# Kernel tuning notes

Measured on AMD Instinct MI355X. Metric: run time of the kernel, lower is better.

Reference implementation:

```python
import jax, jax.numpy as jnp
import numpy as np

H = 1024   # hidden_dim
NH = 16    # num_heads
HD = H // NH  # head_dim = 64
B, S = 2, 2048
LN_EPS = 1e-5


def setup_inputs() -> dict:
    key = jax.random.key(0)
    ks = jax.random.split(key, 5)
    scale = 1.0 / np.sqrt(H)  # xavier-ish scale for stability
    return {
        "x": jax.random.normal(ks[0], (B, S, H), dtype=jnp.float32),
        "Wq": jax.random.normal(ks[1], (H, H), dtype=jnp.float32) * scale,
        "bq": jnp.zeros((H,), jnp.float32),
        "Wk": jax.random.normal(ks[2], (H, H), dtype=jnp.float32) * scale,
        "bk": jnp.zeros((H,), jnp.float32),
        "Wv": jax.random.normal(ks[3], (H, H), dtype=jnp.float32) * scale,
        "bv": jnp.zeros((H,), jnp.float32),
        "Wo": jax.random.normal(ks[4], (H, H), dtype=jnp.float32) * scale,
        "bo": jnp.zeros((H,), jnp.float32),
        "ln_gamma": jnp.ones((H,), jnp.float32),
        "ln_beta": jnp.zeros((H,), jnp.float32),
    }


def reference(x, Wq, bq, Wk, bk, Wv, bv, Wo, bo, ln_gamma, ln_beta):
    b, s, _ = x.shape
    # QKV projections, split heads: (b, nh, s, hd)
    def split_heads(t):
        return t.reshape(b, s, NH, HD).transpose(0, 2, 1, 3)
    Q = split_heads(x @ Wq + bq)
    K = split_heads(x @ Wk + bk)
    V = split_heads(x @ Wv + bv)
    # scaled dot-product with clamp (mask=None path)
    scores = jnp.einsum('bhqd,bhkd->bhqk', Q, K) / np.sqrt(HD).astype(np.float32)
    scores = jnp.clip(scores, -10000.0, 10000.0)
    attn = jax.nn.softmax(scores, axis=-1)
    # dropout is identity in eval mode
    ctx = jnp.einsum('bhqk,bhkd->bhqd', attn, V)
    ctx = ctx.transpose(0, 2, 1, 3).reshape(b, s, H)
    out = ctx @ Wo + bo
    # residual + LayerNorm
    y = out + x
    mu = jnp.mean(y, axis=-1, keepdims=True)
    var = jnp.mean(jnp.square(y - mu), axis=-1, keepdims=True)
    y = (y - mu) * jax.lax.rsqrt(var + LN_EPS)
    return y * ln_gamma + ln_beta
```

## Files before the change

kernel.cpp:

```cpp
#include <hip/hip_runtime.h>

typedef unsigned short u16;
typedef __attribute__((ext_vector_type(8))) short shortx8;
typedef __attribute__((ext_vector_type(4))) float floatx4;
typedef __attribute__((ext_vector_type(2))) unsigned uintx2;

#define GLD16(gp, lp) __builtin_amdgcn_global_load_lds( \
    (__attribute__((address_space(1))) void*)(gp), \
    (__attribute__((address_space(3))) void*)(lp), 16, 0, 0)

__device__ __forceinline__ u16 f2bf(float f) {
  union { float f; unsigned u; } v; v.f = f;
  unsigned r = v.u + 0x7FFFu + ((v.u >> 16) & 1u);
  return (u16)(r >> 16);
}

__device__ __forceinline__ unsigned f2bf_u32(float f) {
  union { float f; unsigned u; } v; v.f = f;
  return (v.u + 0x8000u) >> 16;
}

__global__ __launch_bounds__(256) void cast_x_kernel(const float* __restrict__ x,
                                                     u16* __restrict__ xb, int n4) {
  int i = blockIdx.x * 256 + threadIdx.x;
  if (i < n4) {
    float4 v = ((const float4*)x)[i];
    ushort4 o;
    o.x = f2bf(v.x); o.y = f2bf(v.y); o.z = f2bf(v.z); o.w = f2bf(v.w);
    ((ushort4*)xb)[i] = o;
  }
}

__global__ __launch_bounds__(256) void transpose_cast_w(const float* __restrict__ Wq,
                                                        const float* __restrict__ Wk,
                                                        const float* __restrict__ Wv,
                                                        const float* __restrict__ Wo,
                                                        u16* __restrict__ Wt) {
  __shared__ u16 tile[32][33];
  int mat = blockIdx.z;
  const float* W = (mat == 0) ? Wq : (mat == 1) ? Wk : (mat == 2) ? Wv : Wo;
  u16* dst = Wt + (size_t)mat * 1024 * 1024;
  int n0 = blockIdx.x * 32, k0 = blockIdx.y * 32;
  int tx = threadIdx.x, ty = threadIdx.y;
  for (int i = 0; i < 4; ++i)
    tile[ty + i * 8][tx] = f2bf(W[(size_t)(k0 + ty + i * 8) * 1024 + n0 + tx]);
  __syncthreads();
  for (int i = 0; i < 4; ++i)
    dst[(size_t)(n0 + ty + i * 8) * 1024 + k0 + tx] = tile[tx][ty + i * 8];
}

__device__ __forceinline__ void gemm_tile_core(const u16* __restrict__ A,
                                               const u16* __restrict__ Bt,
                                               int m0, int n0,
                                               u16* As, u16* Bs,
                                               floatx4 (&acc)[4][4]) {
  const int tid = threadIdx.x;
  const int wave = tid >> 6, lane = tid & 63;
  const int lrow = lane >> 4, lcol = lane & 15;
  const int wm = wave >> 1, wn = wave & 1;

  for (int mi = 0; mi < 4; ++mi)
    for (int ni = 0; ni < 4; ++ni)
      acc[mi][ni] = (floatx4){0.f, 0.f, 0.f, 0.f};

  const u16* ap[4];
  const u16* bp[4];
  for (int l = 0; l < 4; ++l) {
    int g = (l * 4 + wave) * 64 + lane;
    int r = g >> 3, c = g & 7;
    int cc = (c ^ (r & 7)) * 8;
    ap[l] = A + (size_t)(m0 + r) * 1024 + cc;
    bp[l] = Bt + (size_t)(n0 + r) * 1024 + cc;
  }

  for (int k0 = 0; k0 < 1024; k0 += 64) {
    __syncthreads();
    for (int l = 0; l < 4; ++l) {
      GLD16(ap[l], As + (l * 4 + wave) * 512);
      GLD16(bp[l], Bs + (l * 4 + wave) * 512);
      ap[l] += 64; bp[l] += 64;
    }
    __syncthreads();
    for (int kk = 0; kk < 2; ++kk) {
      shortx8 af[4], bf[4];
      for (int mi = 0; mi < 4; ++mi) {
        int row = wm * 64 + mi * 16 + lcol;
        int gr = (kk * 4 + lrow) ^ (row & 7);
        af[mi] = *(const shortx8*)&As[row * 64 + gr * 8];
      }
      for (int ni = 0; ni < 4; ++ni) {
        int row = wn * 64 + ni * 16 + lcol;
        int gr = (kk * 4 + lrow) ^ (row & 7);
        bf[ni] = *(const shortx8*)&Bs[row * 64 + gr * 8];
      }
      for (int mi = 0; mi < 4; ++mi)
        for (int ni = 0; ni < 4; ++ni)
          acc[mi][ni] = __builtin_amdgcn_mfma_f32_16x16x32_bf16(af[mi], bf[ni], acc[mi][ni], 0, 0, 0);
    }
  }
}

__global__ __launch_bounds__(256) void qkv_gemm(const u16* __restrict__ xb,
                                                const u16* __restrict__ Wt,
                                                const float* __restrict__ bq,
                                                const float* __restrict__ bk,
                                                const float* __restrict__ bv,
                                                u16* __restrict__ Qh,
                                                u16* __restrict__ Kh,
                                                u16* __restrict__ Vth) {
  __shared__ u16 As[128 * 64];
  __shared__ u16 Bs[128 * 64];
  int m0 = blockIdx.x * 128;
  int mat = blockIdx.y >> 3;
  int n0 = (blockIdx.y & 7) * 128;
  floatx4 acc[4][4];
  gemm_tile_core(xb, Wt + (size_t)mat * 1024 * 1024, m0, n0, As, Bs, acc);

  const float* bias = (mat == 0) ? bq : (mat == 1) ? bk : bv;
  const int tid = threadIdx.x;
  const int wave = tid >> 6, lane = tid & 63;
  const int lrow = lane >> 4, lcol = lane & 15;
  const int wm = wave >> 1, wn = wave & 1;
  const float qscale = 0.18033688011f;

  for (int mi = 0; mi < 4; ++mi) {
    int mbase = m0 + wm * 64 + mi * 16 + lrow * 4;
    for (int ni = 0; ni < 4; ++ni) {
      int n = n0 + wn * 64 + ni * 16 + lcol;
      float bval = bias[n];
      int h = n >> 6, d = n & 63;
      if (mat < 2) {
        u16* dst = (mat == 0) ? Qh : Kh;
        float sc = (mat == 0) ? qscale : 1.0f;
        for (int r = 0; r < 4; ++r) {
          int m = mbase + r;
          int bb = m >> 11, s = m & 2047;
          dst[((size_t)(bb * 16 + h) * 2048 + s) * 64 + d] = f2bf((acc[mi][ni][r] + bval) * sc);
        }
      } else {
        int bb = mbase >> 11, s = mbase & 2047;
        ushort4 pk;
        pk.x = f2bf(acc[mi][ni][0] + bval);
        pk.y = f2bf(acc[mi][ni][1] + bval);
        pk.z = f2bf(acc[mi][ni][2] + bval);
        pk.w = f2bf(acc[mi][ni][3] + bval);
        *(ushort4*)&Vth[((size_t)(bb * 16 + h) * 64 + d) * 2048 + s] = pk;
      }
    }
  }
}

__global__ __launch_bounds__(256) void out_gemm(const u16* __restrict__ ctx,
                                                const u16* __restrict__ Wot,
                                                const float* __restrict__ bo,
                                                float* __restrict__ aout) {
  __shared__ u16 As[128 * 64];
  __shared__ u16 Bs[128 * 64];
  int m0 = blockIdx.x * 128;
  int n0 = blockIdx.y * 128;
  floatx4 acc[4][4];
  gemm_tile_core(ctx, Wot, m0, n0, As, Bs, acc);

  const int tid = threadIdx.x;
  const int wave = tid >> 6, lane = tid & 63;
  const int lrow = lane >> 4, lcol = lane & 15;
  const int wm = wave >> 1, wn = wave & 1;
  for (int mi = 0; mi < 4; ++mi) {
    int mbase = m0 + wm * 64 + mi * 16 + lrow * 4;
    for (int ni = 0; ni < 4; ++ni) {
      int n = n0 + wn * 64 + ni * 16 + lcol;
      float bval = bo[n];
      for (int r = 0; r < 4; ++r)
        aout[(size_t)(mbase + r) * 1024 + n] = acc[mi][ni][r] + bval;
    }
  }
}

__global__ __launch_bounds__(256) void attn_kernel(const u16* __restrict__ Qh,
                                                   const u16* __restrict__ Kh,
                                                   const u16* __restrict__ Vth,
                                                   u16* __restrict__ ctx) {
  __shared__ u16 QPs[64 * 64];
  __shared__ u16 Ks[2][64 * 64];
  __shared__ u16 Vs[2][64 * 64];

  int bh = blockIdx.x;
  int b = bh >> 4, h = bh & 15;
  int q0 = blockIdx.y * 64;
  int tid = threadIdx.x;
  int wave = tid >> 6, lane = tid & 63;
  int lrow = lane >> 4, lcol = lane & 15;

  const u16* Qg = Qh + ((size_t)bh * 2048 + q0) * 64;
  for (int l = 0; l < 2; ++l) {
    int g = (l * 4 + wave) * 64 + lane;
    int r = g >> 3, c = g & 7;
    GLD16(Qg + r * 64 + ((c ^ (r & 7)) * 8), QPs + (l * 4 + wave) * 512);
  }

  const u16* Kbase = Kh + (size_t)bh * 2048 * 64;
  const u16* Vbase = Vth + (size_t)bh * 64 * 2048;

  int gr0[2], gc0[2];
  for (int l = 0; l < 2; ++l) {
    int gg = (l * 4 + wave) * 64 + lane;
    int r = gg >> 3, c = gg & 7;
    gr0[l] = r;
    gc0[l] = (c ^ (r & 7)) * 8;
  }
  for (int l = 0; l < 2; ++l) {
    GLD16(Kbase + (size_t)gr0[l] * 64 + gc0[l], Ks[0] + (l * 4 + wave) * 512);
    GLD16(Vbase + (size_t)gr0[l] * 2048 + gc0[l], Vs[0] + (l * 4 + wave) * 512);
  }
  __syncthreads();

  shortx8 qf[2];
  for (int kk = 0; kk < 2; ++kk) {
    int row = wave * 16 + lcol;
    int gr = (kk * 4 + lrow) ^ (row & 7);
    qf[kk] = *(const shortx8*)&QPs[row * 64 + gr * 8];
  }
  __syncthreads();

  floatx4 o[4];
  float rs = 0.f;
  for (int dt = 0; dt < 4; ++dt) o[dt] = (floatx4){0.f, 0.f, 0.f, 0.f};

  for (int i = 0; i < 32; ++i) {
    int cur = i & 1;
    if (i < 31) {
      int kc = (i + 1) * 64;
      for (int l = 0; l < 2; ++l) {
        GLD16(Kbase + (size_t)(kc + gr0[l]) * 64 + gc0[l], Ks[cur ^ 1] + (l * 4 + wave) * 512);
        GLD16(Vbase + (size_t)gr0[l] * 2048 + kc + gc0[l], Vs[cur ^ 1] + (l * 4 + wave) * 512);
      }
    }

    floatx4 sc[4];
    for (int kt = 0; kt < 4; ++kt)
      sc[kt] = (floatx4){0.f, 0.f, 0.f, 0.f};
    for (int kk = 0; kk < 2; ++kk) {
      for (int kt = 0; kt < 4; ++kt) {
        int row = kt * 16 + lcol;
        int gr = (kk * 4 + lrow) ^ (row & 7);
        shortx8 kf = *(const shortx8*)&Ks[cur][row * 64 + gr * 8];
        sc[kt] = __builtin_amdgcn_mfma_f32_16x16x32_bf16(kf, qf[kk], sc[kt], 0, 0, 0);
      }
    }

    for (int kt = 0; kt < 4; ++kt)
      for (int r = 0; r < 4; ++r) {
        float p = __builtin_amdgcn_exp2f(sc[kt][r]);
        sc[kt][r] = p;
        rs += p;
      }

    {
      int row = wave * 16 + lcol;
      for (int kt = 0; kt < 4; ++kt) {
        int g = kt * 2 + (lrow >> 1);
        int addr = row * 64 + ((g ^ (row & 7)) * 8) + (lrow & 1) * 4;
        uintx2 pk;
        pk.x = f2bf_u32(sc[kt][0]) | (f2bf_u32(sc[kt][1]) << 16);
        pk.y = f2bf_u32(sc[kt][2]) | (f2bf_u32(sc[kt][3]) << 16);
        *(uintx2*)&QPs[addr] = pk;
      }
    }

    for (int kk = 0; kk < 2; ++kk) {
      int prow = wave * 16 + lcol;
      int pgr = (kk * 4 + lrow) ^ (prow & 7);
      shortx8 pf = *(const shortx8*)&QPs[prow * 64 + pgr * 8];
      for (int dt = 0; dt < 4; ++dt) {
        int row = dt * 16 + lcol;
        int gr = (kk * 4 + lrow) ^ (row & 7);
        shortx8 vf = *(const shortx8*)&Vs[cur][row * 64 + gr * 8];
        o[dt] = __builtin_amdgcn_mfma_f32_16x16x32_bf16(vf, pf, o[dt], 0, 0, 0);
      }
    }
    __syncthreads();
  }

  {
    float l = rs;
    l += __shfl_xor(l, 16, 64);
    l += __shfl_xor(l, 32, 64);
    float inv = 1.0f / l;
    int s = q0 + wave * 16 + lcol;
    u16* dst = ctx + (size_t)(b * 2048 + s) * 1024 + h * 64 + lrow * 4;
    for (int dt = 0; dt < 4; ++dt) {
      ushort4 pk;
      pk.x = f2bf(o[dt][0] * inv);
      pk.y = f2bf(o[dt][1] * inv);
      pk.z = f2bf(o[dt][2] * inv);
      pk.w = f2bf(o[dt][3] * inv);
      *(ushort4*)(dst + dt * 16) = pk;
    }
  }
}

__global__ __launch_bounds__(256) void ln_kernel(const float* __restrict__ aout,
                                                 const float* __restrict__ x,
                                                 const float* __restrict__ gamma,
                                                 const float* __restrict__ beta,
                                                 float* __restrict__ out) {
  int row = blockIdx.x;
  int t = threadIdx.x;
  const float4* a4 = (const float4*)(aout + (size_t)row * 1024);
  const float4* x4 = (const float4*)(x + (size_t)row * 1024);
  float4 v = a4[t];
  float4 xv = x4[t];
  v.x += xv.x; v.y += xv.y; v.z += xv.z; v.w += xv.w;
  float s = v.x + v.y + v.z + v.w;
  float s2 = v.x * v.x + v.y * v.y + v.z * v.z + v.w * v.w;
  for (int off = 1; off < 64; off <<= 1) {
    s += __shfl_xor(s, off, 64);
    s2 += __shfl_xor(s2, off, 64);
  }
  __shared__ float red[8];
  int wave = t >> 6, lane = t & 63;
  if (lane == 0) { red[wave] = s; red[4 + wave] = s2; }
  __syncthreads();
  s = red[0] + red[1] + red[2] + red[3];
  s2 = red[4] + red[5] + red[6] + red[7];
  float mu = s * (1.0f / 1024.0f);
  float var = s2 * (1.0f / 1024.0f) - mu * mu;
  float rstd = rsqrtf(var + 1e-5f);
  float4 g = ((const float4*)gamma)[t];
  float4 be = ((const float4*)beta)[t];
  float4 y;
  y.x = (v.x - mu) * rstd * g.x + be.x;
  y.y = (v.y - mu) * rstd * g.y + be.y;
  y.z = (v.z - mu) * rstd * g.z + be.z;
  y.w = (v.w - mu) * rstd * g.w + be.w;
  ((float4*)(out + (size_t)row * 1024))[t] = y;
}

extern "C" void kernel_launch(void* const* d_in, const int* in_sizes, int n_in,
                              void* d_out, int out_size, void* d_ws, size_t ws_size,
                              hipStream_t stream) {
  const float* x     = (const float*)d_in[0];
  const float* Wq    = (const float*)d_in[1];
  const float* bq    = (const float*)d_in[2];
  const float* Wk    = (const float*)d_in[3];
  const float* bk    = (const float*)d_in[4];
  const float* Wv    = (const float*)d_in[5];
  const float* bv    = (const float*)d_in[6];
  const float* Wo    = (const float*)d_in[7];
  const float* bo    = (const float*)d_in[8];
  const float* gamma = (const float*)d_in[9];
  const float* beta  = (const float*)d_in[10];
  float* out = (float*)d_out;

  char* ws = (char*)d_ws;
  u16* xb   = (u16*)(ws);
  u16* Wt   = (u16*)(ws + ((size_t)8 << 20));
  u16* Qh   = (u16*)(ws + ((size_t)16 << 20));
  u16* Kh   = (u16*)(ws + ((size_t)24 << 20));
  u16* Vth  = (u16*)(ws + ((size_t)32 << 20));
  u16* ctx  = (u16*)(ws + ((size_t)40 << 20));
  float* aout = (float*)(ws + ((size_t)48 << 20));

  cast_x_kernel<<<4096, 256, 0, stream>>>(x, xb, 1048576);
  transpose_cast_w<<<dim3(32, 32, 4), dim3(32, 8), 0, stream>>>(Wq, Wk, Wv, Wo, Wt);
  qkv_gemm<<<dim3(32, 24), 256, 0, stream>>>(xb, Wt, bq, bk, bv, Qh, Kh, Vth);
  attn_kernel<<<dim3(32, 32), 256, 0, stream>>>(Qh, Kh, Vth, ctx);
  out_gemm<<<dim3(32, 8), 256, 0, stream>>>(ctx, Wt + (size_t)3 * 1024 * 1024, bo, aout);
  ln_kernel<<<4096, 256, 0, stream>>>(aout, x, gamma, beta, out);
}
```

Baseline: 223.2 us.

## Enlarge attention query tile to 128 rows and narrow out-GEMM N tiles

The attention kernel now uses 512 threads and 128 query rows per block, so each K/V tile loaded into shared memory is reused by twice as many queries, halving K/V global traffic. The out-projection GEMM is rewritten inline with 128x64 tiles, doubling the block count to improve occupancy across CUs. The bf16 packing of probabilities now uses a byte-permute instruction instead of shifts and ORs. The larger attention blocks use more LDS and registers, which can lower residency per CU.

Measured after the change: 207.7 us. 6.9% less time.

```diff
diff --git a/kernel.cpp b/kernel.cpp
--- a/kernel.cpp
+++ b/kernel.cpp
@@ -15,9 +15,9 @@
   return (u16)(r >> 16);
 }
 
-__device__ __forceinline__ unsigned f2bf_u32(float f) {
+__device__ __forceinline__ unsigned bcast_u(float f) {
   union { float f; unsigned u; } v; v.f = f;
-  return (v.u + 0x8000u) >> 16;
+  return v.u;
 }
 
 __global__ __launch_bounds__(256) void cast_x_kernel(const float* __restrict__ x,
@@ -155,20 +155,59 @@
                                                 const float* __restrict__ bo,
                                                 float* __restrict__ aout) {
   __shared__ u16 As[128 * 64];
-  __shared__ u16 Bs[128 * 64];
+  __shared__ u16 Bs[64 * 64];
   int m0 = blockIdx.x * 128;
-  int n0 = blockIdx.y * 128;
-  floatx4 acc[4][4];
-  gemm_tile_core(ctx, Wot, m0, n0, As, Bs, acc);
-
+  int n0 = blockIdx.y * 64;
   const int tid = threadIdx.x;
   const int wave = tid >> 6, lane = tid & 63;
   const int lrow = lane >> 4, lcol = lane & 15;
   const int wm = wave >> 1, wn = wave & 1;
+
+  floatx4 acc[4][2];
+  for (int mi = 0; mi < 4; ++mi)
+    for (int ni = 0; ni < 2; ++ni)
+      acc[mi][ni] = (floatx4){0.f, 0.f, 0.f, 0.f};
+
+  const u16* ap[4];
+  const u16* bp[2];
+  for (int l = 0; l < 4; ++l) {
+    int g = (l * 4 + wave) * 64 + lane;
+    int r = g >> 3, c = g & 7;
+    ap[l] = ctx + (size_t)(m0 + r) * 1024 + (c ^ (r & 7)) * 8;
+  }
+  for (int l = 0; l < 2; ++l) {
+    int g = (l * 4 + wave) * 64 + lane;
+    int r = g >> 3, c = g & 7;
+    bp[l] = Wot + (size_t)(n0 + r) * 1024 + (c ^ (r & 7)) * 8;
+  }
+
+  for (int k0 = 0; k0 < 1024; k0 += 64) {
+    __syncthreads();
+    for (int l = 0; l < 4; ++l) { GLD16(ap[l], As + (l * 4 + wave) * 512); ap[l] += 64; }
+    for (int l = 0; l < 2; ++l) { GLD16(bp[l], Bs + (l * 4 + wave) * 512); bp[l] += 64; }
+    __syncthreads();
+    for (int kk = 0; kk < 2; ++kk) {
+      shortx8 af[4], bf[2];
+      for (int mi = 0; mi < 4; ++mi) {
+        int row = wm * 64 + mi * 16 + lcol;
+        int gr = (kk * 4 + lrow) ^ (row & 7);
+        af[mi] = *(const shortx8*)&As[row * 64 + gr * 8];
+      }
+      for (int ni = 0; ni < 2; ++ni) {
+        int row = wn * 32 + ni * 16 + lcol;
+        int gr = (kk * 4 + lrow) ^ (row & 7);
+        bf[ni] = *(const shortx8*)&Bs[row * 64 + gr * 8];
+      }
+      for (int mi = 0; mi < 4; ++mi)
+        for (int ni = 0; ni < 2; ++ni)
+          acc[mi][ni] = __builtin_amdgcn_mfma_f32_16x16x32_bf16(af[mi], bf[ni], acc[mi][ni], 0, 0, 0);
+    }
+  }
+
   for (int mi = 0; mi < 4; ++mi) {
     int mbase = m0 + wm * 64 + mi * 16 + lrow * 4;
-    for (int ni = 0; ni < 4; ++ni) {
-      int n = n0 + wn * 64 + ni * 16 + lcol;
+    for (int ni = 0; ni < 2; ++ni) {
+      int n = n0 + wn * 32 + ni * 16 + lcol;
       float bval = bo[n];
       for (int r = 0; r < 4; ++r)
         aout[(size_t)(mbase + r) * 1024 + n] = acc[mi][ni][r] + bval;
@@ -176,51 +215,49 @@
   }
 }
 
-__global__ __launch_bounds__(256) void attn_kernel(const u16* __restrict__ Qh,
+__global__ __launch_bounds__(512) void attn_kernel(const u16* __restrict__ Qh,
                                                    const u16* __restrict__ Kh,
                                                    const u16* __restrict__ Vth,
                                                    u16* __restrict__ ctx) {
-  __shared__ u16 QPs[64 * 64];
+  __shared__ u16 QPs[128 * 64];
   __shared__ u16 Ks[2][64 * 64];
   __shared__ u16 Vs[2][64 * 64];
 
   int bh = blockIdx.x;
   int b = bh >> 4, h = bh & 15;
-  int q0 = blockIdx.y * 64;
+  int q0 = blockIdx.y * 128;
   int tid = threadIdx.x;
   int wave = tid >> 6, lane = tid & 63;
   int lrow = lane >> 4, lcol = lane & 15;
 
   const u16* Qg = Qh + ((size_t)bh * 2048 + q0) * 64;
   for (int l = 0; l < 2; ++l) {
-    int g = (l * 4 + wave) * 64 + lane;
+    int g = (l * 8 + wave) * 64 + lane;
     int r = g >> 3, c = g & 7;
-    GLD16(Qg + r * 64 + ((c ^ (r & 7)) * 8), QPs + (l * 4 + wave) * 512);
+    GLD16(Qg + r * 64 + ((c ^ (r & 7)) * 8), QPs + (l * 8 + wave) * 512);
   }
 
   const u16* Kbase = Kh + (size_t)bh * 2048 * 64;
   const u16* Vbase = Vth + (size_t)bh * 64 * 2048;
 
-  int gr0[2], gc0[2];
-  for (int l = 0; l < 2; ++l) {
-    int gg = (l * 4 + wave) * 64 + lane;
-    int r = gg >> 3, c = gg & 7;
-    gr0[l] = r;
-    gc0[l] = (c ^ (r & 7)) * 8;
-  }
-  for (int l = 0; l < 2; ++l) {
-    GLD16(Kbase + (size_t)gr0[l] * 64 + gc0[l], Ks[0] + (l * 4 + wave) * 512);
-    GLD16(Vbase + (size_t)gr0[l] * 2048 + gc0[l], Vs[0] + (l * 4 + wave) * 512);
-  }
+  int g = wave * 64 + lane;
+  int gr = g >> 3, gc = g & 7;
+  int cc = (gc ^ (gr & 7)) * 8;
+  const u16* kp = Kbase + (size_t)gr * 64 + cc;
+  const u16* vp = Vbase + (size_t)gr * 2048 + cc;
+
+  GLD16(kp, (u16*)Ks + wave * 512);
+  GLD16(vp, (u16*)Vs + wave * 512);
+  kp += 4096;
+  vp += 64;
   __syncthreads();
 
   shortx8 qf[2];
   for (int kk = 0; kk < 2; ++kk) {
     int row = wave * 16 + lcol;
-    int gr = (kk * 4 + lrow) ^ (row & 7);
-    qf[kk] = *(const shortx8*)&QPs[row * 64 + gr * 8];
-  }
-  __syncthreads();
+    int grr = (kk * 4 + lrow) ^ (row & 7);
+    qf[kk] = *(const shortx8*)&QPs[row * 64 + grr * 8];
+  }
 
   floatx4 o[4];
   float rs = 0.f;
@@ -229,11 +266,10 @@
   for (int i = 0; i < 32; ++i) {
     int cur = i & 1;
     if (i < 31) {
-      int kc = (i + 1) * 64;
-      for (int l = 0; l < 2; ++l) {
-        GLD16(Kbase + (size_t)(kc + gr0[l]) * 64 + gc0[l], Ks[cur ^ 1] + (l * 4 + wave) * 512);
-        GLD16(Vbase + (size_t)gr0[l] * 2048 + kc + gc0[l], Vs[cur ^ 1] + (l * 4 + wave) * 512);
-      }
+      GLD16(kp, (u16*)Ks + (cur ^ 1) * 4096 + wave * 512);
+      GLD16(vp, (u16*)Vs + (cur ^ 1) * 4096 + wave * 512);
+      kp += 4096;
+      vp += 64;
     }
 
     floatx4 sc[4];
@@ -242,8 +278,8 @@
     for (int kk = 0; kk < 2; ++kk) {
       for (int kt = 0; kt < 4; ++kt) {
         int row = kt * 16 + lcol;
-        int gr = (kk * 4 + lrow) ^ (row & 7);
-        shortx8 kf = *(const shortx8*)&Ks[cur][row * 64 + gr * 8];
+        int grr = (kk * 4 + lrow) ^ (row & 7);
+        shortx8 kf = *(const shortx8*)&Ks[cur][row * 64 + grr * 8];
         sc[kt] = __builtin_amdgcn_mfma_f32_16x16x32_bf16(kf, qf[kk], sc[kt], 0, 0, 0);
       }
     }
@@ -258,11 +294,15 @@
     {
       int row = wave * 16 + lcol;
       for (int kt = 0; kt < 4; ++kt) {
-        int g = kt * 2 + (lrow >> 1);
-        int addr = row * 64 + ((g ^ (row & 7)) * 8) + (lrow & 1) * 4;
+        int gg = kt * 2 + (lrow >> 1);
+        int addr = row * 64 + ((gg ^ (row & 7)) * 8) + (lrow & 1) * 4;
+        unsigned t0 = bcast_u(sc[kt][0]) + 0x8000u;
+        unsigned t1 = bcast_u(sc[kt][1]) + 0x8000u;
+        unsigned t2 = bcast_u(sc[kt][2]) + 0x8000u;
+        unsigned t3 = bcast_u(sc[kt][3]) + 0x8000u;
         uintx2 pk;
-        pk.x = f2bf_u32(sc[kt][0]) | (f2bf_u32(sc[kt][1]) << 16);
-        pk.y = f2bf_u32(sc[kt][2]) | (f2bf_u32(sc[kt][3]) << 16);
+        pk.x = __builtin_amdgcn_perm(t1, t0, 0x07060302u);
+        pk.y = __builtin_amdgcn_perm(t3, t2, 0x07060302u);
         *(uintx2*)&QPs[addr] = pk;
       }
     }
@@ -273,8 +313,8 @@
       shortx8 pf = *(const shortx8*)&QPs[prow * 64 + pgr * 8];
       for (int dt = 0; dt < 4; ++dt) {
         int row = dt * 16 + lcol;
-        int gr = (kk * 4 + lrow) ^ (row & 7);
-        shortx8 vf = *(const shortx8*)&Vs[cur][row * 64 + gr * 8];
+        int grr = (kk * 4 + lrow) ^ (row & 7);
+        shortx8 vf = *(const shortx8*)&Vs[cur][row * 64 + grr * 8];
         o[dt] = __builtin_amdgcn_mfma_f32_16x16x32_bf16(vf, pf, o[dt], 0, 0, 0);
       }
     }
@@ -364,7 +404,7 @@
   cast_x_kernel<<<4096, 256, 0, stream>>>(x, xb, 1048576);
   transpose_cast_w<<<dim3(32, 32, 4), dim3(32, 8), 0, stream>>>(Wq, Wk, Wv, Wo, Wt);
   qkv_gemm<<<dim3(32, 24), 256, 0, stream>>>(xb, Wt, bq, bk, bv, Qh, Kh, Vth);
-  attn_kernel<<<dim3(32, 32), 256, 0, stream>>>(Qh, Kh, Vth, ctx);
-  out_gemm<<<dim3(32, 8), 256, 0, stream>>>(ctx, Wt + (size_t)3 * 1024 * 1024, bo, aout);
+  attn_kernel<<<dim3(32, 16), 512, 0, stream>>>(Qh, Kh, Vth, ctx);
+  out_gemm<<<dim3(32, 16), 256, 0, stream>>>(ctx, Wt + (size_t)3 * 1024 * 1024, bo, aout);
   ln_kernel<<<4096, 256, 0, stream>>>(aout, x, gamma, beta, out);
 }
```
